# Optimization experiments

Measured on AMD Instinct MI355X. Metric: run time of the kernel, lower is better.

The kernel has to match this reference:

```python
import jax, jax.numpy as jnp
import numpy as np

B, L, DIM, H, HD = 1, 2048, 3072, 24, 128
RANK, ALPHA, LORA_WEIGHT = 16, 16.0, 1.0
LORA_SCALE = ALPHA / RANK * LORA_WEIGHT


def _rope_pe(seq_len, head_dim, theta=10000.0):
    # Flux rope: pe[l, d/2, 2, 2] rotation matrices, returned as [1,1,L,d/2,2,2]
    pos = jnp.arange(seq_len, dtype=jnp.float32)
    omega = 1.0 / (theta ** (jnp.arange(0, head_dim, 2, dtype=jnp.float32) / head_dim))
    ang = pos[:, None] * omega[None, :]                      # [L, HD/2]
    cos, sin = jnp.cos(ang), jnp.sin(ang)
    pe = jnp.stack([jnp.stack([cos, -sin], -1),
                    jnp.stack([sin, cos], -1)], -2)          # [L, HD/2, 2, 2]
    return pe[None, None]                                    # [1,1,L,HD/2,2,2]


def setup_inputs() -> dict:
    key = jax.random.key(0)
    ks = jax.random.split(key, 8)
    std = 0.02
    return {
        "x": jax.random.normal(ks[0], (B, L, DIM), jnp.float32),
        "pe": _rope_pe(L, HD),
        "qkv_w": jax.random.normal(ks[1], (3 * DIM, DIM), jnp.float32) * std,
        "qkv_b": jnp.zeros((3 * DIM,), jnp.float32),
        "proj_w": jax.random.normal(ks[2], (DIM, DIM), jnp.float32) * std,
        "proj_b": jnp.zeros((DIM,), jnp.float32),
        # torch init: down ~ N(0, 1/rank); up is zeros at init but we use small randn
        # so the LoRA path is numerically active for kernel testing.
        "qkv_down": jax.random.normal(ks[3], (RANK, DIM), jnp.float32) / RANK,
        "qkv_up": jax.random.normal(ks[4], (3 * DIM, RANK), jnp.float32) * std,
        "proj_down": jax.random.normal(ks[5], (RANK, DIM), jnp.float32) / RANK,
        "proj_up": jax.random.normal(ks[6], (DIM, RANK), jnp.float32) * std,
        "q_scale": jnp.ones((HD,), jnp.float32),
        "k_scale": jnp.ones((HD,), jnp.float32),
    }


def _rmsnorm(t, scale):
    # Flux QKNorm: per-head RMSNorm with learned scale over head_dim
    return t * jax.lax.rsqrt(jnp.mean(t * t, axis=-1, keepdims=True) + 1e-6) * scale


def _apply_rope(t, pe):
    # t: [B,H,L,HD]; pe: [1,1,L,HD/2,2,2]; out[...,i] = pe[...,i,0]*t0 + pe[...,i,1]*t1
    t2 = t.reshape(*t.shape[:-1], HD // 2, 2)
    out = jnp.einsum('...ij,...j->...i', pe, t2)
    return out.reshape(t.shape)


def reference(x, pe, qkv_w, qkv_b, proj_w, proj_b,
              qkv_down, qkv_up, proj_down, proj_up, q_scale, k_scale):
    # fused qkv + LoRA epilogue
    qkv = x @ qkv_w.T + qkv_b + ((x @ qkv_down.T) @ qkv_up.T) * LORA_SCALE
    qkv = qkv.reshape(B, L, 3, H, HD).transpose(2, 0, 3, 1, 4)  # [3,B,H,L,HD]
    q, k, v = qkv[0], qkv[1], qkv[2]
    q = _rmsnorm(q, q_scale)
    k = _rmsnorm(k, k_scale)
    q = _apply_rope(q, pe)
    k = _apply_rope(k, pe)
    scores = jnp.einsum('bhqd,bhkd->bhqk', q, k) / jnp.sqrt(jnp.float32(HD))
    p = jax.nn.softmax(scores, axis=-1)
    o = jnp.einsum('bhqk,bhkd->bhqd', p, v)
    o = o.transpose(0, 2, 1, 3).reshape(B, L, H * HD)           # B L (H D)
    # output proj + LoRA epilogue
    out = o @ proj_w.T + proj_b + ((o @ proj_down.T) @ proj_up.T) * LORA_SCALE
    return out
```

## Files before the change

### kernel.cpp

```cpp
#include <hip/hip_runtime.h>
#include <math.h>

#define L_SEQ 2048
#define DIM   3072
#define NH    24
#define HD    128
#define RANK  16
#define N_QKV 9216
#define KE    3136

typedef __attribute__((ext_vector_type(8))) short bf16x8;
typedef __attribute__((ext_vector_type(4))) float f32x4;
typedef unsigned short u16;
typedef unsigned int u32;

__device__ __forceinline__ u16 f2bf(float f) {
    union { float f; u32 u; } v; v.f = f;
    return (u16)((v.u + 0x7fffu + ((v.u >> 16) & 1u)) >> 16);
}
__device__ __forceinline__ float bf2f(u16 h) {
    union { u32 u; float f; } v; v.u = ((u32)h) << 16; return v.f;
}

#define GLOBAL_TO_LDS16(gp, lp) \
  __builtin_amdgcn_global_load_lds((const __attribute__((address_space(1))) u32*)(gp), \
                                   (__attribute__((address_space(3))) u32*)(lp), 16, 0, 0)

__global__ __launch_bounds__(64) void pack_pe_kernel(
    const float* __restrict__ pe, float2* __restrict__ pe2)
{
    int l = blockIdx.x, i = threadIdx.x;
    int base = l * 256 + i * 4;
    float2 cs; cs.x = pe[base]; cs.y = pe[base + 2];
    pe2[l * 64 + i] = cs;
}

__global__ __launch_bounds__(256) void lora_down_kernel(
    const float* __restrict__ X, const float* __restrict__ W, float* __restrict__ T)
{
    int l = blockIdx.x;
    int r = threadIdx.x >> 4;
    int lane = threadIdx.x & 15;
    const float* xr = X + (size_t)l * DIM;
    const float* wr = W + (size_t)r * DIM;
    float s = 0.f;
    for (int k = lane; k < DIM; k += 16) s = fmaf(xr[k], wr[k], s);
    #pragma unroll
    for (int mm = 8; mm; mm >>= 1) s += __shfl_xor(s, mm);
    if (lane == 0) T[l * RANK + r] = s;
}

__global__ __launch_bounds__(256) void lora_down_bf_kernel(
    const u16* __restrict__ X, const float* __restrict__ W, float* __restrict__ T, int pitch)
{
    int l = blockIdx.x;
    int r = threadIdx.x >> 4;
    int lane = threadIdx.x & 15;
    const u16* xr = X + (size_t)l * pitch;
    const float* wr = W + (size_t)r * DIM;
    float s = 0.f;
    for (int k = lane; k < DIM; k += 16) s = fmaf(bf2f(xr[k]), wr[k], s);
    #pragma unroll
    for (int mm = 8; mm; mm >>= 1) s += __shfl_xor(s, mm);
    if (lane == 0) T[l * RANK + r] = s;
}

__global__ __launch_bounds__(256) void pack_w_kernel(
    const float* __restrict__ W, const float* __restrict__ Up, u16* __restrict__ out)
{
    int row = blockIdx.x;
    const float* wr = W + (size_t)row * DIM;
    u16* orow = out + (size_t)row * KE;
    #pragma unroll
    for (int it = 0; it < 3; it++) {
        int c4 = threadIdx.x + it * 256;
        float4 v = ((const float4*)wr)[c4];
        ushort4 o = {f2bf(v.x), f2bf(v.y), f2bf(v.z), f2bf(v.w)};
        *(ushort4*)(orow + c4 * 4) = o;
    }
    int t = threadIdx.x;
    if (t < RANK) {
        u16 b = f2bf(Up[row * RANK + t]);
        orow[DIM + t] = b;
        orow[DIM + RANK + t] = b;
    } else if (t >= 32 && t < 64) {
        orow[DIM + t] = 0;
    }
}

__global__ __launch_bounds__(256) void pack_x_kernel(
    const float* __restrict__ X, const float* __restrict__ T, u16* __restrict__ out)
{
    int row = blockIdx.x;
    const float* xr = X + (size_t)row * DIM;
    u16* orow = out + (size_t)row * KE;
    #pragma unroll
    for (int it = 0; it < 3; it++) {
        int c4 = threadIdx.x + it * 256;
        float4 v = ((const float4*)xr)[c4];
        ushort4 o = {f2bf(v.x), f2bf(v.y), f2bf(v.z), f2bf(v.w)};
        *(ushort4*)(orow + c4 * 4) = o;
    }
    int t = threadIdx.x;
    if (t < RANK) {
        float tv = T[row * RANK + t];
        u16 hi = f2bf(tv);
        orow[DIM + t] = hi;
        orow[DIM + RANK + t] = f2bf(tv - bf2f(hi));
    } else if (t >= 32 && t < 64) {
        orow[DIM + t] = 0;
    }
}

__global__ __launch_bounds__(64) void pack_t_kernel(
    const float* __restrict__ T, u16* __restrict__ out)
{
    int row = blockIdx.x, t = threadIdx.x;
    u16* orow = out + (size_t)row * KE;
    if (t < RANK) {
        float tv = T[row * RANK + t];
        u16 hi = f2bf(tv);
        orow[DIM + t] = hi;
        orow[DIM + RANK + t] = f2bf(tv - bf2f(hi));
    } else if (t >= 32) {
        orow[DIM + t] = 0;
    }
}

template<int MODE>
__global__ __launch_bounds__(256) void gemm_mfma_kernel(
    const u16* __restrict__ A, const u16* __restrict__ W,
    const float* __restrict__ bias,
    float* __restrict__ Cf,
    u16* __restrict__ qkbf, u16* __restrict__ vT,
    const float2* __restrict__ pe2,
    const float* __restrict__ q_scale, const float* __restrict__ k_scale,
    int M, int N, int K)
{
    __shared__ __align__(16) u16 a_s[128 * 64];
    __shared__ __align__(16) u16 b_s[128 * 64];

    int tid = threadIdx.x;
    int wave = tid >> 6, lane = tid & 63;
    int quad = lane >> 4, l15 = lane & 15;
    int wm = wave >> 1, wn = wave & 1;

    int num_n = N >> 7;
    int xcd = blockIdx.x & 7;
    int loc = blockIdx.x >> 3;
    int bm = (((xcd & 3) << 2) + (loc & 3)) << 7;
    int bn = ((xcd >> 2) * (num_n >> 1) + (loc >> 2)) << 7;

    const u16* ga[4]; const u16* gb[4];
    u16 *lA[4], *lB[4];
    #pragma unroll
    for (int e = 0; e < 4; e++) {
        int r = e * 32 + (tid >> 3);
        int g = (tid & 7) ^ (r & 7);
        ga[e] = A + (size_t)(bm + r) * K + g * 8;
        gb[e] = W + (size_t)(bn + r) * K + g * 8;
        lA[e] = &a_s[(e * 32 + wave * 8) * 64];
        lB[e] = &b_s[(e * 32 + wave * 8) * 64];
    }

    f32x4 acc[4][4];
    #pragma unroll
    for (int i = 0; i < 4; i++)
        #pragma unroll
        for (int j = 0; j < 4; j++) acc[i][j] = (f32x4){0.f, 0.f, 0.f, 0.f};

    int abase[4], bbase[4], co[2];
    #pragma unroll
    for (int i = 0; i < 4; i++) {
        abase[i] = (wm * 64 + i * 16 + l15) * 64;
        bbase[i] = (wn * 64 + i * 16 + l15) * 64;
    }
    #pragma unroll
    for (int ks = 0; ks < 2; ks++) co[ks] = ((ks * 4 + quad) ^ (l15 & 7)) * 8;

    for (int k0 = 0; k0 < K; k0 += 64) {
        #pragma unroll
        for (int e = 0; e < 4; e++) {
            GLOBAL_TO_LDS16(ga[e] + k0, lA[e]);
            GLOBAL_TO_LDS16(gb[e] + k0, lB[e]);
        }
        __syncthreads();
        #pragma unroll
        for (int ks = 0; ks < 2; ks++) {
            bf16x8 af[4], bf[4];
            #pragma unroll
            for (int i = 0; i < 4; i++) af[i] = *(const bf16x8*)&a_s[abase[i] + co[ks]];
            #pragma unroll
            for (int j = 0; j < 4; j++) bf[j] = *(const bf16x8*)&b_s[bbase[j] + co[ks]];
            #pragma unroll
            for (int i = 0; i < 4; i++)
                #pragma unroll
                for (int j = 0; j < 4; j++)
                    acc[i][j] = __builtin_amdgcn_mfma_f32_16x16x32_bf16(af[i], bf[j], acc[i][j], 0, 0, 0);
        }
        __syncthreads();
    }

    if (MODE == 0) {
        #pragma unroll
        for (int j = 0; j < 4; j++) {
            int col = bn + wn * 64 + j * 16 + l15;
            float bj = bias[col];
            #pragma unroll
            for (int i = 0; i < 4; i++)
                #pragma unroll
                for (int r = 0; r < 4; r++) {
                    int row = bm + wm * 64 + i * 16 + quad * 4 + r;
                    Cf[(size_t)row * N + col] = acc[i][j][r] + bj;
                }
        }
        return;
    }

    int tn = bn >> 7;
    int mq = (tn >= 48) ? 2 : (tn >= 24 ? 1 : 0);
    int h = tn - mq * 24;

    #pragma unroll
    for (int j = 0; j < 4; j++) {
        float bj = bias[bn + wn * 64 + j * 16 + l15];
        #pragma unroll
        for (int i = 0; i < 4; i++)
            #pragma unroll
            for (int r = 0; r < 4; r++) acc[i][j][r] += bj;
    }

    if (mq == 2) {
        #pragma unroll
        for (int j = 0; j < 4; j++) {
            int d = wn * 64 + j * 16 + l15;
            u16* vrow = vT + ((size_t)h * HD + d) * L_SEQ;
            #pragma unroll
            for (int i = 0; i < 4; i++)
                #pragma unroll
                for (int r = 0; r < 4; r++) {
                    int kv = bm + wm * 64 + i * 16 + quad * 4 + r;
                    int slot = ((kv >> 3) & 7) ^ (d & 7);
                    int colp = (kv & ~63) + slot * 8 + (kv & 7);
                    vrow[colp] = f2bf(acc[i][j][r]);
                }
        }
    } else {
        float ssp[4][4];
        #pragma unroll
        for (int i = 0; i < 4; i++)
            #pragma unroll
            for (int r = 0; r < 4; r++) {
                float s = 0.f;
                #pragma unroll
                for (int j = 0; j < 4; j++) s = fmaf(acc[i][j][r], acc[i][j][r], s);
                #pragma unroll
                for (int mm = 8; mm; mm >>= 1) s += __shfl_xor(s, mm);
                ssp[i][r] = s;
            }
        float* ss_s = (float*)a_s;
        if (l15 == 0) {
            #pragma unroll
            for (int i = 0; i < 4; i++)
                *(float4*)&ss_s[wn * 128 + wm * 64 + i * 16 + quad * 4] =
                    make_float4(ssp[i][0], ssp[i][1], ssp[i][2], ssp[i][3]);
        }
        __syncthreads();
        float rfac[4][4];
        #pragma unroll
        for (int i = 0; i < 4; i++) {
            float4 s0 = *(const float4*)&ss_s[wm * 64 + i * 16 + quad * 4];
            float4 s1 = *(const float4*)&ss_s[128 + wm * 64 + i * 16 + quad * 4];
            rfac[i][0] = rsqrtf((s0.x + s1.x) * (1.f / HD) + 1e-6f);
            rfac[i][1] = rsqrtf((s0.y + s1.y) * (1.f / HD) + 1e-6f);
            rfac[i][2] = rsqrtf((s0.z + s1.z) * (1.f / HD) + 1e-6f);
            rfac[i][3] = rsqrtf((s0.w + s1.w) * (1.f / HD) + 1e-6f);
        }
        const float* scale = mq ? k_scale : q_scale;
        float sgn = (l15 & 1) ? 1.f : -1.f;
        u16* obase = qkbf + (size_t)(mq * NH + h) * L_SEQ * HD;
        #pragma unroll
        for (int j = 0; j < 4; j++) {
            int d = wn * 64 + j * 16 + l15;
            float sd = scale[d];
            #pragma unroll
            for (int i = 0; i < 4; i++)
                #pragma unroll
                for (int r = 0; r < 4; r++) {
                    int row = bm + wm * 64 + i * 16 + quad * 4 + r;
                    float t = acc[i][j][r] * rfac[i][r] * sd;
                    float tp = __shfl_xor(t, 1);
                    float2 cs = pe2[row * 64 + (d >> 1)];
                    float o = fmaf(cs.x, t, sgn * cs.y * tp);
                    obase[(size_t)row * HD + d] = f2bf(o);
                }
        }
    }
}

__global__ __launch_bounds__(256) void attn_mfma_kernel(
    const u16* __restrict__ qk_bf, const u16* __restrict__ vT, u16* __restrict__ Og)
{
    __shared__ __align__(16) u16 k_s[64 * 128];
    __shared__ __align__(16) u16 v_s[128 * 64];
    __shared__ __align__(16) u16 p_s[4][16 * 72];

    int bid = blockIdx.x;
    int loc = bid >> 3;
    int h = (bid & 7) * 3 + (loc >> 5);
    int q0 = (loc & 31) * 64;
    int tid = threadIdx.x;
    int wave = tid >> 6, lane = tid & 63;
    int quad = lane >> 4, l15 = lane & 15;
    const u16* qb = qk_bf + (size_t)h * L_SEQ * HD;
    const u16* kb = qk_bf + (size_t)(NH + h) * L_SEQ * HD;
    const u16* vTh = vT + (size_t)h * HD * L_SEQ;

    bf16x8 aq[4];
    {
        const u16* qr = qb + (size_t)(q0 + wave * 16 + l15) * HD + quad * 8;
        #pragma unroll
        for (int ks = 0; ks < 4; ks++) aq[ks] = *(const bf16x8*)(qr + ks * 32);
    }

    f32x4 o_acc[8];
    #pragma unroll
    for (int n = 0; n < 8; n++) o_acc[n] = (f32x4){0.f, 0.f, 0.f, 0.f};
    float lsum[4] = {0.f, 0.f, 0.f, 0.f};
    const float sc = 0.08838834764831845f * 1.4426950408889634f;
    const float MB = 64.0f;

    const u16* gk[4];
    #pragma unroll
    for (int e = 0; e < 4; e++) {
        int r = wave * 16 + e * 4 + (lane >> 4);
        int g = l15 ^ (r & 15);
        gk[e] = kb + (size_t)r * HD + g * 8;
    }
    const u16* gv[4];
    #pragma unroll
    for (int e = 0; e < 4; e++) {
        int d = wave * 32 + e * 8 + (lane >> 3);
        gv[e] = vTh + (size_t)d * L_SEQ + (lane & 7) * 8;
    }
    int vco[2];
    #pragma unroll
    for (int ks = 0; ks < 2; ks++) vco[ks] = ((ks * 4 + quad) ^ (l15 & 7)) * 8;

    for (int kv0 = 0; kv0 < L_SEQ; kv0 += 64) {
        __syncthreads();
        #pragma unroll
        for (int e = 0; e < 4; e++) {
            GLOBAL_TO_LDS16(gk[e] + (size_t)kv0 * HD, &k_s[(wave * 16 + e * 4) * 128]);
            GLOBAL_TO_LDS16(gv[e] + kv0, &v_s[(wave * 32 + e * 8) * 64]);
        }
        __syncthreads();

        f32x4 sacc[4];
        #pragma unroll
        for (int j = 0; j < 4; j++) sacc[j] = (f32x4){0.f, 0.f, 0.f, 0.f};
        #pragma unroll
        for (int ks = 0; ks < 4; ks++) {
            #pragma unroll
            for (int j = 0; j < 4; j++) {
                int n = j * 16 + l15;
                int slot = (ks * 4 + quad) ^ (n & 15);
                bf16x8 bk = *(const bf16x8*)&k_s[n * 128 + slot * 8];
                sacc[j] = __builtin_amdgcn_mfma_f32_16x16x32_bf16(aq[ks], bk, sacc[j], 0, 0, 0);
            }
        }

        #pragma unroll
        for (int j = 0; j < 4; j++)
            #pragma unroll
            for (int r = 0; r < 4; r++) {
                float p = exp2f(fmaf(sacc[j][r], sc, -MB));
                sacc[j][r] = p;
                lsum[r] += p;
                p_s[wave][(quad * 4 + r) * 72 + j * 16 + l15] = f2bf(p);
            }
        bf16x8 ap[2];
        #pragma unroll
        for (int ks = 0; ks < 2; ks++)
            ap[ks] = *(const bf16x8*)&p_s[wave][l15 * 72 + ks * 32 + quad * 8];

        #pragma unroll
        for (int ks = 0; ks < 2; ks++) {
            #pragma unroll
            for (int n = 0; n < 8; n++) {
                bf16x8 bv = *(const bf16x8*)&v_s[(n * 16 + l15) * 64 + vco[ks]];
                o_acc[n] = __builtin_amdgcn_mfma_f32_16x16x32_bf16(ap[ks], bv, o_acc[n], 0, 0, 0);
            }
        }
    }

    #pragma unroll
    for (int r = 0; r < 4; r++) {
        #pragma unroll
        for (int mm = 8; mm; mm >>= 1) lsum[r] += __shfl_xor(lsum[r], mm);
    }

    #pragma unroll
    for (int r = 0; r < 4; r++) {
        float inv = 1.f / lsum[r];
        int row = q0 + wave * 16 + quad * 4 + r;
        u16* orow = Og + (size_t)row * KE + h * HD;
        #pragma unroll
        for (int n = 0; n < 8; n++)
            orow[n * 16 + l15] = f2bf(o_acc[n][r] * inv);
    }
}

extern "C" void kernel_launch(void* const* d_in, const int* in_sizes, int n_in,
                              void* d_out, int out_size, void* d_ws, size_t ws_size,
                              hipStream_t stream)
{
    const float* x         = (const float*)d_in[0];
    const float* pe        = (const float*)d_in[1];
    const float* qkv_w     = (const float*)d_in[2];
    const float* qkv_b     = (const float*)d_in[3];
    const float* proj_w    = (const float*)d_in[4];
    const float* proj_b    = (const float*)d_in[5];
    const float* qkv_down  = (const float*)d_in[6];
    const float* qkv_up    = (const float*)d_in[7];
    const float* proj_down = (const float*)d_in[8];
    const float* proj_up   = (const float*)d_in[9];
    const float* q_scale   = (const float*)d_in[10];
    const float* k_scale   = (const float*)d_in[11];
    float* out = (float*)d_out;

    char* w = (char*)d_ws;
    u16*   qk_bf  = (u16*)w;    w += (size_t)2 * NH * L_SEQ * HD * 2;
    u16*   vT_bf  = (u16*)w;    w += (size_t)NH * HD * L_SEQ * 2;
    u16*   x_ext  = (u16*)w;    w += (size_t)L_SEQ * KE * 2;
    u16*   wq_ext = (u16*)w;    w += (size_t)N_QKV * KE * 2;
    u16*   wp_ext = (u16*)w;    w += (size_t)DIM * KE * 2;
    u16*   o_ext  = (u16*)w;    w += (size_t)L_SEQ * KE * 2;
    float2* pe2   = (float2*)w; w += (size_t)L_SEQ * 64 * sizeof(float2);
    float* t1     = (float*)w;  w += (size_t)L_SEQ * RANK * 4;
    float* t2     = (float*)w;

    pack_pe_kernel<<<L_SEQ, 64, 0, stream>>>(pe, pe2);
    pack_w_kernel<<<N_QKV, 256, 0, stream>>>(qkv_w, qkv_up, wq_ext);
    pack_w_kernel<<<DIM, 256, 0, stream>>>(proj_w, proj_up, wp_ext);
    lora_down_kernel<<<L_SEQ, 256, 0, stream>>>(x, qkv_down, t1);
    pack_x_kernel<<<L_SEQ, 256, 0, stream>>>(x, t1, x_ext);

    gemm_mfma_kernel<1><<<(N_QKV / 128) * (L_SEQ / 128), 256, 0, stream>>>(
        x_ext, wq_ext, qkv_b, nullptr, qk_bf, vT_bf, pe2, q_scale, k_scale,
        L_SEQ, N_QKV, KE);
    attn_mfma_kernel<<<(L_SEQ / 64) * NH, 256, 0, stream>>>(qk_bf, vT_bf, o_ext);
    lora_down_bf_kernel<<<L_SEQ, 256, 0, stream>>>(o_ext, proj_down, t2, KE);
    pack_t_kernel<<<L_SEQ, 64, 0, stream>>>(t2, o_ext);
    gemm_mfma_kernel<0><<<(DIM / 128) * (L_SEQ / 128), 256, 0, stream>>>(
        o_ext, wp_ext, proj_b, out, nullptr, nullptr, nullptr, nullptr, nullptr,
        L_SEQ, DIM, KE);
}
```

Before: 715.3 us.

## Double-buffer LDS tiles in MFMA GEMM to overlap global loads with compute

Doubles the shared-memory A/B tiles and prefetches the next K-tile directly into LDS while MFMAs run on the current one. The barrier now sits once per iteration after a vmcnt wait instead of twice, and compute is wrapped in s_setprio. The aim is to hide global-load latency in the QKV and projection GEMMs. It costs twice the LDS (64KB), which may lower occupancy.

```diff
diff --git a/kernel.cpp b/kernel.cpp
--- a/kernel.cpp
+++ b/kernel.cpp
@@ -137,8 +137,8 @@
     const float* __restrict__ q_scale, const float* __restrict__ k_scale,
     int M, int N, int K)
 {
-    __shared__ __align__(16) u16 a_s[128 * 64];
-    __shared__ __align__(16) u16 b_s[128 * 64];
+    __shared__ __align__(16) u16 a_s[2][128 * 64];
+    __shared__ __align__(16) u16 b_s[2][128 * 64];
 
     int tid = threadIdx.x;
     int wave = tid >> 6, lane = tid & 63;
@@ -159,8 +159,8 @@
         int g = (tid & 7) ^ (r & 7);
         ga[e] = A + (size_t)(bm + r) * K + g * 8;
         gb[e] = W + (size_t)(bn + r) * K + g * 8;
-        lA[e] = &a_s[(e * 32 + wave * 8) * 64];
-        lB[e] = &b_s[(e * 32 + wave * 8) * 64];
+        lA[e] = &a_s[0][(e * 32 + wave * 8) * 64];
+        lB[e] = &b_s[0][(e * 32 + wave * 8) * 64];
     }
 
     f32x4 acc[4][4];
@@ -178,27 +178,44 @@
     #pragma unroll
     for (int ks = 0; ks < 2; ks++) co[ks] = ((ks * 4 + quad) ^ (l15 & 7)) * 8;
 
-    for (int k0 = 0; k0 < K; k0 += 64) {
-        #pragma unroll
-        for (int e = 0; e < 4; e++) {
-            GLOBAL_TO_LDS16(ga[e] + k0, lA[e]);
-            GLOBAL_TO_LDS16(gb[e] + k0, lB[e]);
-        }
-        __syncthreads();
+    #pragma unroll
+    for (int e = 0; e < 4; e++) {
+        GLOBAL_TO_LDS16(ga[e], lA[e]);
+        GLOBAL_TO_LDS16(gb[e], lB[e]);
+    }
+    asm volatile("s_waitcnt vmcnt(0)" ::: "memory");
+    __builtin_amdgcn_s_barrier();
+
+    int nt = K >> 6;
+    for (int t = 0; t < nt; ++t) {
+        int cur = t & 1;
+        int cb = cur * 8192;
+        int nb = (cur ^ 1) * 8192;
+        if (t + 1 < nt) {
+            int ko = (t + 1) << 6;
+            #pragma unroll
+            for (int e = 0; e < 4; e++) {
+                GLOBAL_TO_LDS16(ga[e] + ko, lA[e] + nb);
+                GLOBAL_TO_LDS16(gb[e] + ko, lB[e] + nb);
+            }
+        }
+        __builtin_amdgcn_s_setprio(1);
         #pragma unroll
         for (int ks = 0; ks < 2; ks++) {
             bf16x8 af[4], bf[4];
             #pragma unroll
-            for (int i = 0; i < 4; i++) af[i] = *(const bf16x8*)&a_s[abase[i] + co[ks]];
-            #pragma unroll
-            for (int j = 0; j < 4; j++) bf[j] = *(const bf16x8*)&b_s[bbase[j] + co[ks]];
+            for (int i = 0; i < 4; i++) af[i] = *(const bf16x8*)&a_s[0][cb + abase[i] + co[ks]];
+            #pragma unroll
+            for (int j = 0; j < 4; j++) bf[j] = *(const bf16x8*)&b_s[0][cb + bbase[j] + co[ks]];
             #pragma unroll
             for (int i = 0; i < 4; i++)
                 #pragma unroll
                 for (int j = 0; j < 4; j++)
                     acc[i][j] = __builtin_amdgcn_mfma_f32_16x16x32_bf16(af[i], bf[j], acc[i][j], 0, 0, 0);
         }
-        __syncthreads();
+        __builtin_amdgcn_s_setprio(0);
+        asm volatile("s_waitcnt vmcnt(0)" ::: "memory");
+        __builtin_amdgcn_s_barrier();
     }
 
     if (MODE == 0) {
```

Result: faster. 689.4 us (-3.6%).
